# Optimization experiments

Hardware: AMD Instinct MI355X
Metric: run time of the kernel (lower is better)

Reference implementation:

```python
import jax, jax.numpy as jnp
import numpy as np

N_FOOD = 50000
N_NUT = 50000
E = 800000
D = 128      # embedding_dim == hidden_dim
H = 4        # heads
C = D // H   # per-head channels
L = 2        # num_layers
NEG_SLOPE = 0.2


def _gat_conv(x_src, x_dst, ei, Wsrc, Wdst, a_src, a_dst, bias, n_dst):
    """PyG GATConv (bipartite, no self loops, concat heads, no edge_dim)."""
    hs = (x_src @ Wsrc).reshape(-1, H, C)   # [Ns, H, C]
    hd = (x_dst @ Wdst).reshape(-1, H, C)   # [Nd, H, C]
    src, dst = ei[0], ei[1]
    alpha_s = jnp.einsum('nhc,hc->nh', hs, a_src)  # [Ns, H]
    alpha_d = jnp.einsum('nhc,hc->nh', hd, a_dst)  # [Nd, H]
    e = alpha_s[src] + alpha_d[dst]                # [E, H]
    e = jax.nn.leaky_relu(e, NEG_SLOPE)
    # segment softmax over edges grouped by destination node
    emax = jax.ops.segment_max(e, dst, num_segments=n_dst)
    emax = jnp.where(jnp.isfinite(emax), emax, 0.0)
    ex = jnp.exp(e - emax[dst])
    denom = jax.ops.segment_sum(ex, dst, num_segments=n_dst)
    alpha = ex / (denom[dst] + 1e-16)              # [E, H]
    msg = hs[src] * alpha[:, :, None]              # [E, H, C]
    out = jax.ops.segment_sum(msg, dst, num_segments=n_dst)
    return out.reshape(n_dst, H * C) + bias


def setup_inputs() -> dict:
    key = jax.random.key(0)
    ks = jax.random.split(key, 16)
    w = 1.0 / np.sqrt(D)
    a = 1.0 / np.sqrt(C)
    inp = {
        'x_food': jax.random.normal(ks[0], (N_FOOD, D), jnp.float32),
        'x_nut': jax.random.normal(ks[1], (N_NUT, D), jnp.float32),
        'Wsrc_fn': jax.random.normal(ks[2], (L, D, D), jnp.float32) * w,
        'Wdst_fn': jax.random.normal(ks[3], (L, D, D), jnp.float32) * w,
        'att_src_fn': jax.random.normal(ks[4], (L, H, C), jnp.float32) * a,
        'att_dst_fn': jax.random.normal(ks[5], (L, H, C), jnp.float32) * a,
        'bias_fn': jnp.zeros((L, D), jnp.float32),
        'Wsrc_nf': jax.random.normal(ks[6], (L, D, D), jnp.float32) * w,
        'Wdst_nf': jax.random.normal(ks[7], (L, D, D), jnp.float32) * w,
        'att_src_nf': jax.random.normal(ks[8], (L, H, C), jnp.float32) * a,
        'att_dst_nf': jax.random.normal(ks[9], (L, H, C), jnp.float32) * a,
        'bias_nf': jnp.zeros((L, D), jnp.float32),
        'ei_fn': jax.random.randint(ks[10], (2, E), 0, N_FOOD, jnp.int32),  # food -> nutrient
        'ei_nf': jax.random.randint(ks[11], (2, E), 0, N_NUT, jnp.int32),   # nutrient -> food
    }
    return inp


def reference(x_food, x_nut, Wsrc_fn, Wdst_fn, att_src_fn, att_dst_fn, bias_fn,
              Wsrc_nf, Wdst_nf, att_src_nf, att_dst_nf, bias_nf, ei_fn, ei_nf):
    h_food, h_nut = x_food, x_nut
    for l in range(L):
        # relation food --contains--> nutrient (dst = nutrient)
        out_nut = _gat_conv(h_food, h_nut, ei_fn, Wsrc_fn[l], Wdst_fn[l],
                            att_src_fn[l], att_dst_fn[l], bias_fn[l], N_NUT)
        # relation nutrient --contained_in--> food (dst = food)
        out_food = _gat_conv(h_nut, h_food, ei_nf, Wsrc_nf[l], Wdst_nf[l],
                             att_src_nf[l], att_dst_nf[l], bias_nf[l], N_FOOD)
        # dropout is identity at inference; ELU activation
        h_food = jax.nn.elu(out_food)
        h_nut = jax.nn.elu(out_nut)
    return jnp.stack([h_food, h_nut])  # [2, 50000, 128]
```

## Files before the change

### kernel.cpp

```cpp
#include <hip/hip_runtime.h>
#include <math.h>

#define NNODE 50000
#define NEDGE 800000
#define DIM   128
#define NHEAD 4
#define NTILE ((NNODE + 63) / 64)
#define NBUCK 196
#define ECHUNK 196
#define CAP   6144
#define LOG2E 1.44269504088896340736f

typedef __bf16 bf16x8 __attribute__((ext_vector_type(8)));
typedef float  f32x4  __attribute__((ext_vector_type(4)));
typedef float  f32x2  __attribute__((ext_vector_type(2)));

static __device__ __forceinline__ void bfsplit(float x, ushort& hi, ushort& lo) {
    __bf16 h = (__bf16)x;
    float hf = (float)h;
    __bf16 l = (__bf16)(x - hf);
    hi = __builtin_bit_cast(unsigned short, h);
    lo = __builtin_bit_cast(unsigned short, l);
}
static __device__ __forceinline__ ushort f2h(float x) {
    _Float16 h = (_Float16)x;
    return __builtin_bit_cast(unsigned short, h);
}
static __device__ __forceinline__ f32x2 up2v(unsigned u) {
    f32x2 r;
    r.x = (float)__builtin_bit_cast(_Float16, (unsigned short)(u & 0xffff));
    r.y = (float)__builtin_bit_cast(_Float16, (unsigned short)(u >> 16));
    return r;
}
static __device__ __forceinline__ unsigned encf(float f) {
    unsigned u = __builtin_bit_cast(unsigned, f);
    return (u >> 31) ? ~u : (u | 0x80000000u);
}
static __device__ __forceinline__ float decf(unsigned x) {
    unsigned u = (x >> 31) ? (x & 0x7fffffffu) : ~x;
    return __builtin_bit_cast(float, u);
}

__global__ __launch_bounds__(256) void bhist(const int* __restrict__ eA,
                                             const int* __restrict__ eB,
                                             int* __restrict__ bcnt) {
    int rel = (int)(blockIdx.x >= ECHUNK);
    const int* dstrow = (rel ? eB : eA) + NEDGE;
    int blk = blockIdx.x - rel * ECHUNK;
    __shared__ int hist[256];
    hist[threadIdx.x] = 0;
    __syncthreads();
    int base = blk * 4096;
    #pragma unroll
    for (int k = 0; k < 16; k++) {
        int e = base + k * 256 + threadIdx.x;
        if (e < NEDGE) atomicAdd(&hist[dstrow[e] >> 8], 1);
    }
    __syncthreads();
    int h = hist[threadIdx.x];
    if (h) atomicAdd(&bcnt[rel * 256 + threadIdx.x], h);
}

__global__ __launch_bounds__(256) void bscan(const int* __restrict__ bcnt,
                                             int* __restrict__ bko, int* __restrict__ bcur,
                                             int* __restrict__ ptrA, int* __restrict__ ptrB) {
    int rel = blockIdx.x;
    __shared__ int tmp[256];
    int t = threadIdx.x;
    int v = bcnt[rel * 256 + t];
    tmp[t] = v; __syncthreads();
    for (int off = 1; off < 256; off <<= 1) {
        int a = (t >= off) ? tmp[t - off] : 0; __syncthreads();
        tmp[t] += a; __syncthreads();
    }
    int excl = tmp[t] - v;
    bko[rel * 256 + t] = excl;
    bcur[rel * 256 + t] = excl;
    if (t == 255) (rel ? ptrB : ptrA)[NNODE] = tmp[255];
}

__global__ __launch_bounds__(256) void bscatter(const int* __restrict__ eA,
                                                const int* __restrict__ eB,
                                                int* __restrict__ bcur,
                                                unsigned* __restrict__ bktA,
                                                unsigned* __restrict__ bktB) {
    int rel = (int)(blockIdx.x >= ECHUNK);
    const int* ebase = rel ? eB : eA;
    unsigned* bkt = rel ? bktB : bktA;
    int blk = blockIdx.x - rel * ECHUNK;
    __shared__ int hist[256], bas[256], cur[256];
    hist[threadIdx.x] = 0;
    __syncthreads();
    int base = blk * 4096;
    #pragma unroll
    for (int k = 0; k < 16; k++) {
        int e = base + k * 256 + threadIdx.x;
        if (e < NEDGE) atomicAdd(&hist[ebase[NEDGE + e] >> 8], 1);
    }
    __syncthreads();
    int h = hist[threadIdx.x];
    bas[threadIdx.x] = h ? atomicAdd(&bcur[rel * 256 + threadIdx.x], h) : 0;
    cur[threadIdx.x] = 0;
    __syncthreads();
    #pragma unroll
    for (int k = 0; k < 16; k++) {
        int e = base + k * 256 + threadIdx.x;
        if (e < NEDGE) {
            int s = ebase[e], d = ebase[NEDGE + e];
            int b = d >> 8;
            int loc = atomicAdd(&cur[b], 1);
            bkt[bas[b] + loc] = ((unsigned)(d & 255) << 16) | (unsigned)s;
        }
    }
}

__global__ __launch_bounds__(256) void bsort(const unsigned* __restrict__ bktA,
                                             const unsigned* __restrict__ bktB,
                                             const int* __restrict__ bko,
                                             int* __restrict__ ptrA, int* __restrict__ ptrB,
                                             ushort* __restrict__ srcA, ushort* __restrict__ srcB) {
    int rel = (int)(blockIdx.x >= NBUCK);
    const unsigned* bkt = rel ? bktB : bktA;
    int* ptr   = rel ? ptrB : ptrA;
    ushort* srcs = rel ? srcB : srcA;
    int b = blockIdx.x - rel * NBUCK;
    int beg = bko[rel * 256 + b], end = bko[rel * 256 + b + 1];
    int cnt_e = end - beg;
    __shared__ int hist[256], excl[256], cur[256];
    __shared__ unsigned sorted[CAP];
    int t = threadIdx.x;
    hist[t] = 0;
    __syncthreads();
    for (int i = t; i < cnt_e; i += 256) atomicAdd(&hist[bkt[beg + i] >> 16], 1);
    __syncthreads();
    int v = hist[t];
    excl[t] = v; __syncthreads();
    for (int off = 1; off < 256; off <<= 1) {
        int a = (t >= off) ? excl[t - off] : 0; __syncthreads();
        excl[t] += a; __syncthreads();
    }
    int ex = excl[t] - v;
    int d = b * 256 + t;
    if (d < NNODE) ptr[d] = beg + ex;
    cur[t] = ex;
    __syncthreads();
    for (int i = t; i < cnt_e; i += 256) {
        unsigned u = bkt[beg + i];
        int dl = u >> 16;
        int p = atomicAdd(&cur[dl], 1);
        if (p < CAP) sorted[p] = u;
        else srcs[beg + p] = (ushort)(u & 0xffffu);
    }
    __syncthreads();
    int lim = cnt_e < CAP ? cnt_e : CAP;
    for (int i = t; i < lim; i += 256) {
        unsigned u = sorted[i];
        srcs[beg + i] = (ushort)(u & 0xffffu);
    }
}

__global__ void prep_wav(const float* __restrict__ Wsrc_fn, const float* __restrict__ a_src_fn,
                         const float* __restrict__ Wdst_fn, const float* __restrict__ a_dst_fn,
                         const float* __restrict__ Wsrc_nf, const float* __restrict__ a_src_nf,
                         const float* __restrict__ Wdst_nf, const float* __restrict__ a_dst_nf,
                         float* __restrict__ wav) {
    int call = blockIdx.x;
    int layer = call >> 1, which = call & 1;
    const float* Ws = which ? Wsrc_nf : Wsrc_fn;
    const float* as = which ? a_src_nf : a_src_fn;
    const float* Wd = which ? Wdst_fn : Wdst_nf;
    const float* ad = which ? a_dst_fn : a_dst_nf;
    Ws += layer * DIM * DIM; Wd += layer * DIM * DIM;
    as += layer * DIM; ad += layer * DIM;
    for (int it = threadIdx.x; it < 512; it += 256) {
        int k = it >> 2, h = it & 3;
        float s = 0.f, dv = 0.f;
        #pragma unroll 8
        for (int c = 0; c < 32; c++) {
            s  += Ws[k * DIM + h * 32 + c] * as[h * 32 + c];
            dv += Wd[k * DIM + h * 32 + c] * ad[h * 32 + c];
        }
        float* o = wav + (size_t)call * DIM * 8 + k * 8;
        o[h] = s; o[h + 4] = dv;
    }
}

__global__ __launch_bounds__(256, 3) void transform_kernel(
    const float* __restrict__ XA, const float* __restrict__ WA, const float* __restrict__ wavA,
    ushort* __restrict__ HSA, float* __restrict__ ASA, float* __restrict__ ADA,
    const float* __restrict__ XB, const float* __restrict__ WB, const float* __restrict__ wavB,
    ushort* __restrict__ HSB, float* __restrict__ ASB, float* __restrict__ ADB,
    unsigned* __restrict__ Mg, int nb)
{
    int rel = (int)(blockIdx.x >= (unsigned)nb);
    const float* X  = rel ? XB : XA;
    const float* W  = rel ? WB : WA;
    const float* wav = rel ? wavB : wavA;
    ushort* HS = rel ? HSB : HSA;
    float*  AS = rel ? ASB : ASA;
    float*  AD = rel ? ADB : ADA;

    __shared__ ushort WTh[64][136], WTl[64][136];
    __shared__ ushort wavTh[16][136], wavTl[16][136];
    __shared__ ushort hsb[64][72];
    __shared__ unsigned mloc[4];

    int vb = blockIdx.x - rel * nb;
    int half = vb & 1;
    int ch = half * 64;

    for (int i = threadIdx.x; i < 64 * DIM; i += 256) {
        int col = i & 63, k = i >> 6;
        ushort hi, lo; bfsplit(W[k * DIM + ch + col], hi, lo);
        WTh[col][k] = hi; WTl[col][k] = lo;
    }
    if (half == 0) {
        for (int i = threadIdx.x; i < 16 * DIM; i += 256) {
            int c = i & 15, k = i >> 4;
            float w = (c < 8) ? wav[k * 8 + c] : 0.f;
            ushort hi, lo; bfsplit(w, hi, lo);
            wavTh[c][k] = hi; wavTl[c][k] = lo;
        }
    }
    if (threadIdx.x < 4) mloc[threadIdx.x] = 0;
    __syncthreads();

    const int wv = threadIdx.x >> 6, lane = threadIdx.x & 63;
    const int lm = lane & 15, lq = lane >> 4;
    const int r0 = wv * 16;
    const int tstride = nb >> 1;

    auto loadX = [&](int tile, float4* dst) {
        int myrow = tile * 64 + r0 + lm;
        int rowc = myrow < NNODE ? myrow : NNODE - 1;
        const float4* Xr = (const float4*)(X + (size_t)rowc * DIM);
        #pragma unroll
        for (int kc = 0; kc < 4; kc++) {
            dst[kc * 2]     = Xr[kc * 8 + lq * 2];
            dst[kc * 2 + 1] = Xr[kc * 8 + lq * 2 + 1];
        }
    };

    auto computeTile = [&](const float4* xv, int tile) {
        int row0 = tile * 64;
        f32x4 acc[4] = {{0,0,0,0},{0,0,0,0},{0,0,0,0},{0,0,0,0}};
        f32x4 accv = {0,0,0,0};
        #pragma unroll
        for (int kc = 0; kc < 4; kc++) {
            const float* fp = (const float*)&xv[kc * 2];
            bf16x8 ah, al;
            #pragma unroll
            for (int j = 0; j < 8; j++) {
                float x = fp[j];
                __bf16 h = (__bf16)x;
                ah[j] = h;
                al[j] = (__bf16)(x - (float)h);
            }
            int k0 = kc * 32 + lq * 8;
            #pragma unroll
            for (int ct = 0; ct < 4; ct++) {
                bf16x8 bh = *(const bf16x8*)&WTh[ct * 16 + lm][k0];
                bf16x8 bl = *(const bf16x8*)&WTl[ct * 16 + lm][k0];
                acc[ct] = __builtin_amdgcn_mfma_f32_16x16x32_bf16(al, bh, acc[ct], 0, 0, 0);
                acc[ct] = __builtin_amdgcn_mfma_f32_16x16x32_bf16(ah, bl, acc[ct], 0, 0, 0);
                acc[ct] = __builtin_amdgcn_mfma_f32_16x16x32_bf16(ah, bh, acc[ct], 0, 0, 0);
            }
            if (half == 0) {
                bf16x8 vh = *(const bf16x8*)&wavTh[lm][k0];
                bf16x8 vl = *(const bf16x8*)&wavTl[lm][k0];
                accv = __builtin_amdgcn_mfma_f32_16x16x32_bf16(al, vh, accv, 0, 0, 0);
                accv = __builtin_amdgcn_mfma_f32_16x16x32_bf16(ah, vl, accv, 0, 0, 0);
                accv = __builtin_amdgcn_mfma_f32_16x16x32_bf16(ah, vh, accv, 0, 0, 0);
            }
        }

        if (half == 0 && lm < 8) {
            accv *= LOG2E;
            float mx4 = -INFINITY;
            #pragma unroll
            for (int r = 0; r < 4; r++) {
                int row = row0 + r0 + lq * 4 + r;
                if (row < NNODE) {
                    if (lm < 4) AS[row * 4 + lm] = accv[r];
                    else        AD[row * 4 + (lm - 4)] = accv[r];
                }
                mx4 = fmaxf(mx4, accv[r]);
            }
            if (lm < 4) atomicMax(&mloc[lm], encf(mx4));
        }

        __syncthreads();
        #pragma unroll
        for (int ct = 0; ct < 4; ct++) {
            #pragma unroll
            for (int r = 0; r < 4; r++)
                hsb[r0 + lq * 4 + r][ct * 16 + lm] = f2h(acc[ct][r]);
        }
        __syncthreads();
        #pragma unroll
        for (int p = 0; p < 2; p++) {
            int idx = p * 256 + (int)threadIdx.x;
            int lr = idx >> 3, off = (idx & 7) * 8;
            int rg = row0 + lr;
            if (rg < NNODE)
                *(uint4*)(HS + (size_t)rg * DIM + ch + off) = *(const uint4*)&hsb[lr][off];
        }
    };

    float4 xa[8], xb[8];
    int tile = vb >> 1;
    loadX(tile, xa);
    while (tile < NTILE) {
        if (tile + tstride < NTILE) loadX(tile + tstride, xb);
        computeTile(xa, tile);
        tile += tstride;
        if (tile >= NTILE) break;
        if (tile + tstride < NTILE) loadX(tile + tstride, xa);
        computeTile(xb, tile);
        tile += tstride;
    }

    __syncthreads();
    if (half == 0 && threadIdx.x < 4)
        atomicMax(&Mg[rel * 4 + threadIdx.x], mloc[threadIdx.x]);
}

__global__ __launch_bounds__(256) void agg_kernel(
    const ushort* __restrict__ HSA, const float* __restrict__ ASA, const float* __restrict__ ADA,
    const int* __restrict__ ptrA, const ushort* __restrict__ srcA,
    const float* __restrict__ biasA, float* __restrict__ outA,
    const ushort* __restrict__ HSB, const float* __restrict__ ASB, const float* __restrict__ ADB,
    const int* __restrict__ ptrB, const ushort* __restrict__ srcB,
    const float* __restrict__ biasB, float* __restrict__ outB,
    const unsigned* __restrict__ Mg, int nb)
{
    int rel = (int)(blockIdx.x >= (unsigned)nb);
    const uint4* HS4 = (const uint4*)(rel ? HSB : HSA);
    const float* AS = rel ? ASB : ASA;
    const float* AD = rel ? ADB : ADA;
    const ushort* srcs = rel ? srcB : srcA;
    const int* ptr = rel ? ptrB : ptrA;
    const float* bias = rel ? biasB : biasA;
    float* out = rel ? outB : outA;

    int bid = blockIdx.x - rel * nb;
    int wave = threadIdx.x >> 6, lane = threadIdx.x & 63;
    int d = bid * 4 + wave;
    if (d >= NNODE) return;

    int q  = lane >> 4;
    int li = lane & 15;
    int hh = li >> 2;

    float ad_h = AD[d * 4 + hh];
    float mm = decf(Mg[rel * 4 + hh]) + ad_h;
    mm = mm > 0.f ? mm : 0.2f * mm;

    int e0 = ptr[d], e1 = ptr[d + 1];

    float acc[8] = {0.f,0.f,0.f,0.f,0.f,0.f,0.f,0.f};
    float l = 0.f;

    int e = e0;
    for (; e + 8 <= e1; e += 8) {
        int iA = e + q, iB = e + 4 + q;
        int sA = srcs[iA], sB = srcs[iB];
        uint4 hA = HS4[sA * 16 + li];
        uint4 hB = HS4[sB * 16 + li];
        float aA = AS[sA * 4 + hh];
        float aB = AS[sB * 4 + hh];
        float vA = aA + ad_h; vA = fmaxf(vA, 0.2f * vA);
        float vB = aB + ad_h; vB = fmaxf(vB, 0.2f * vB);
        float pA = __builtin_amdgcn_exp2f(vA - mm);
        float pB = __builtin_amdgcn_exp2f(vB - mm);
        l += pA + pB;
        #pragma unroll
        for (int j = 0; j < 4; j++) {
            f32x2 h2A = up2v(((const unsigned*)&hA)[j]);
            f32x2 h2B = up2v(((const unsigned*)&hB)[j]);
            acc[2*j]   += h2A.x * pA + h2B.x * pB;
            acc[2*j+1] += h2A.y * pA + h2B.y * pB;
        }
    }
    for (; e < e1; e += 4) {
        int ee = e + q;
        bool act = ee < e1;
        int eidx = act ? ee : e1 - 1;
        int s = srcs[eidx];
        uint4 hv = HS4[s * 16 + li];
        float av = AS[s * 4 + hh];
        float v = av + ad_h; v = fmaxf(v, 0.2f * v);
        float p = __builtin_amdgcn_exp2f(v - mm);
        p = act ? p : 0.f;
        l += p;
        #pragma unroll
        for (int j = 0; j < 4; j++) {
            f32x2 h2 = up2v(((const unsigned*)&hv)[j]);
            acc[2*j]   += h2.x * p;
            acc[2*j+1] += h2.y * p;
        }
    }

    #pragma unroll
    for (int j = 0; j < 8; j++) {
        acc[j] += __shfl_xor(acc[j], 16, 64);
        acc[j] += __shfl_xor(acc[j], 32, 64);
    }
    l += __shfl_xor(l, 16, 64);
    l += __shfl_xor(l, 32, 64);

    if (q == 0) {
        float inv = 1.f / (l + 1e-16f);
        const float4* b4 = (const float4*)bias + li * 2;
        float4 b0 = b4[0], b1 = b4[1];
        float o[8];
        o[0] = acc[0] * inv + b0.x; o[1] = acc[1] * inv + b0.y;
        o[2] = acc[2] * inv + b0.z; o[3] = acc[3] * inv + b0.w;
        o[4] = acc[4] * inv + b1.x; o[5] = acc[5] * inv + b1.y;
        o[6] = acc[6] * inv + b1.z; o[7] = acc[7] * inv + b1.w;
        #pragma unroll
        for (int j = 0; j < 8; j++)
            o[j] = o[j] > 0.f ? o[j] : __expf(o[j]) - 1.f;
        float4* o4 = (float4*)(out + (size_t)d * DIM) + li * 2;
        o4[0] = make_float4(o[0], o[1], o[2], o[3]);
        o4[1] = make_float4(o[4], o[5], o[6], o[7]);
    }
}

extern "C" void kernel_launch(void* const* d_in, const int* in_sizes, int n_in,
                              void* d_out, int out_size, void* d_ws, size_t ws_size,
                              hipStream_t stream) {
    const float* x_food      = (const float*)d_in[0];
    const float* x_nut       = (const float*)d_in[1];
    const float* Wsrc_fn     = (const float*)d_in[2];
    const float* Wdst_fn     = (const float*)d_in[3];
    const float* att_src_fn  = (const float*)d_in[4];
    const float* att_dst_fn  = (const float*)d_in[5];
    const float* bias_fn     = (const float*)d_in[6];
    const float* Wsrc_nf     = (const float*)d_in[7];
    const float* Wdst_nf     = (const float*)d_in[8];
    const float* att_src_nf  = (const float*)d_in[9];
    const float* att_dst_nf  = (const float*)d_in[10];
    const float* bias_nf     = (const float*)d_in[11];
    const int*   ei_fn       = (const int*)d_in[12];
    const int*   ei_nf       = (const int*)d_in[13];
    float* out = (float*)d_out;

    char* ws = (char*)d_ws;
    size_t off = 0;
    auto alloc_f = [&](size_t n) { float* p = (float*)(ws + off); off += n * 4; return p; };
    auto alloc_i = [&](size_t n) { int* p = (int*)(ws + off); off += n * 4; return p; };
    auto alloc_u = [&](size_t n) { ushort* p = (ushort*)(ws + off); off += n * 2; return p; };

    float* B_food = alloc_f((size_t)NNODE * DIM);
    float* B_nut  = alloc_f((size_t)NNODE * DIM);
    ushort* HS_fn = alloc_u((size_t)NNODE * DIM);
    ushort* HS_nf = alloc_u((size_t)NNODE * DIM);
    float* AS_fn  = alloc_f(NNODE * NHEAD);
    float* AS_nf  = alloc_f(NNODE * NHEAD);
    float* AD_fn  = alloc_f(NNODE * NHEAD);
    float* AD_nf  = alloc_f(NNODE * NHEAD);
    float* wav    = alloc_f(4 * DIM * 8);
    int* ptr_fn   = alloc_i(50004);
    int* ptr_nf   = alloc_i(50004);
    ushort* srcs_fn = alloc_u(NEDGE);
    ushort* srcs_nf = alloc_u(NEDGE);
    int* bcnt     = alloc_i(512);
    unsigned* Mbuf = (unsigned*)alloc_i(16);
    int* bko      = alloc_i(512);
    int* bcur     = alloc_i(512);
    unsigned* bkt_fn = (unsigned*)B_food;
    unsigned* bkt_nf = (unsigned*)B_nut;

    hipMemsetAsync(bcnt, 0, (512 + 16) * 4, stream);
    bhist<<<2 * ECHUNK, 256, 0, stream>>>(ei_fn, ei_nf, bcnt);
    bscan<<<2, 256, 0, stream>>>(bcnt, bko, bcur, ptr_fn, ptr_nf);
    bscatter<<<2 * ECHUNK, 256, 0, stream>>>(ei_fn, ei_nf, bcur, bkt_fn, bkt_nf);
    bsort<<<2 * NBUCK, 256, 0, stream>>>(bkt_fn, bkt_nf, bko, ptr_fn, ptr_nf,
                                         srcs_fn, srcs_nf);

    prep_wav<<<4, 256, 0, stream>>>(Wsrc_fn, att_src_fn, Wdst_fn, att_dst_fn,
                                    Wsrc_nf, att_src_nf, Wdst_nf, att_dst_nf, wav);

    const int WL = DIM * DIM;
    const int TNB = 384;
    const int ANB = (NNODE + 3) / 4;
    float* wav0 = wav;
    float* wav1 = wav + DIM * 8;
    float* wav2 = wav + 2 * DIM * 8;
    float* wav3 = wav + 3 * DIM * 8;

    transform_kernel<<<2 * TNB, 256, 0, stream>>>(
        x_food, Wsrc_fn, wav0, HS_fn, AS_fn, AD_nf,
        x_nut,  Wsrc_nf, wav1, HS_nf, AS_nf, AD_fn, Mbuf, TNB);
    agg_kernel<<<2 * ANB, 256, 0, stream>>>(
        HS_fn, AS_fn, AD_fn, ptr_fn, srcs_fn, bias_fn, B_nut,
        HS_nf, AS_nf, AD_nf, ptr_nf, srcs_nf, bias_nf, B_food, Mbuf, ANB);

    transform_kernel<<<2 * TNB, 256, 0, stream>>>(
        B_food, Wsrc_fn + WL, wav2, HS_fn, AS_fn, AD_nf,
        B_nut,  Wsrc_nf + WL, wav3, HS_nf, AS_nf, AD_fn, Mbuf + 8, TNB);
    agg_kernel<<<2 * ANB, 256, 0, stream>>>(
        HS_fn, AS_fn, AD_fn, ptr_fn, srcs_fn, bias_fn + DIM, out + (size_t)NNODE * DIM,
        HS_nf, AS_nf, AD_nf, ptr_nf, srcs_nf, bias_nf + DIM, out, Mbuf + 8, ANB);
}
```

Before: 356.7 us.

## Split aggregation across two half-feature blocks and trim transform shared memory

The aggregation kernel now splits each destination node's 128 features into two 64-channel halves handled by separate interleaved blocks. Each wave processes 8 edges per step instead of 4, with native f16x8 conversion and FMA accumulation. The transform kernel moves the attention-vector weights from LDS into registers and halves the hsb staging buffer by writing it in two passes, which allows 4 blocks per CU and a larger grid. The split doubles gather traffic for edge indices and attention scalars and adds more barriers in the transform store path.

```diff
diff --git a/kernel.cpp b/kernel.cpp
--- a/kernel.cpp
+++ b/kernel.cpp
@@ -10,10 +10,12 @@
 #define ECHUNK 196
 #define CAP   6144
 #define LOG2E 1.44269504088896340736f
+#define NODEBLK 12500
 
 typedef __bf16 bf16x8 __attribute__((ext_vector_type(8)));
 typedef float  f32x4  __attribute__((ext_vector_type(4)));
 typedef float  f32x2  __attribute__((ext_vector_type(2)));
+typedef _Float16 f16x8 __attribute__((ext_vector_type(8)));
 
 static __device__ __forceinline__ void bfsplit(float x, ushort& hi, ushort& lo) {
     __bf16 h = (__bf16)x;
@@ -25,12 +27,6 @@
 static __device__ __forceinline__ ushort f2h(float x) {
     _Float16 h = (_Float16)x;
     return __builtin_bit_cast(unsigned short, h);
-}
-static __device__ __forceinline__ f32x2 up2v(unsigned u) {
-    f32x2 r;
-    r.x = (float)__builtin_bit_cast(_Float16, (unsigned short)(u & 0xffff));
-    r.y = (float)__builtin_bit_cast(_Float16, (unsigned short)(u >> 16));
-    return r;
 }
 static __device__ __forceinline__ unsigned encf(float f) {
     unsigned u = __builtin_bit_cast(unsigned, f);
@@ -185,7 +181,7 @@
     }
 }
 
-__global__ __launch_bounds__(256, 3) void transform_kernel(
+__global__ __launch_bounds__(256, 4) void transform_kernel(
     const float* __restrict__ XA, const float* __restrict__ WA, const float* __restrict__ wavA,
     ushort* __restrict__ HSA, float* __restrict__ ASA, float* __restrict__ ADA,
     const float* __restrict__ XB, const float* __restrict__ WB, const float* __restrict__ wavB,
@@ -201,8 +197,7 @@
     float*  AD = rel ? ADB : ADA;
 
     __shared__ ushort WTh[64][136], WTl[64][136];
-    __shared__ ushort wavTh[16][136], wavTl[16][136];
-    __shared__ ushort hsb[64][72];
+    __shared__ ushort hsb[32][72];
     __shared__ unsigned mloc[4];
 
     int vb = blockIdx.x - rel * nb;
@@ -214,21 +209,28 @@
         ushort hi, lo; bfsplit(W[k * DIM + ch + col], hi, lo);
         WTh[col][k] = hi; WTl[col][k] = lo;
     }
-    if (half == 0) {
-        for (int i = threadIdx.x; i < 16 * DIM; i += 256) {
-            int c = i & 15, k = i >> 4;
-            float w = (c < 8) ? wav[k * 8 + c] : 0.f;
-            ushort hi, lo; bfsplit(w, hi, lo);
-            wavTh[c][k] = hi; wavTl[c][k] = lo;
-        }
-    }
     if (threadIdx.x < 4) mloc[threadIdx.x] = 0;
-    __syncthreads();
 
     const int wv = threadIdx.x >> 6, lane = threadIdx.x & 63;
     const int lm = lane & 15, lq = lane >> 4;
     const int r0 = wv * 16;
     const int tstride = nb >> 1;
+
+    bf16x8 wvh[4], wvl[4];
+    if (half == 0) {
+        #pragma unroll
+        for (int kc = 0; kc < 4; kc++) {
+            int k0 = kc * 32 + lq * 8;
+            #pragma unroll
+            for (int j = 0; j < 8; j++) {
+                float w = (lm < 8) ? wav[(k0 + j) * 8 + lm] : 0.f;
+                __bf16 h = (__bf16)w;
+                wvh[kc][j] = h;
+                wvl[kc][j] = (__bf16)(w - (float)h);
+            }
+        }
+    }
+    __syncthreads();
 
     auto loadX = [&](int tile, float4* dst) {
         int myrow = tile * 64 + r0 + lm;
@@ -266,11 +268,9 @@
                 acc[ct] = __builtin_amdgcn_mfma_f32_16x16x32_bf16(ah, bh, acc[ct], 0, 0, 0);
             }
             if (half == 0) {
-                bf16x8 vh = *(const bf16x8*)&wavTh[lm][k0];
-                bf16x8 vl = *(const bf16x8*)&wavTl[lm][k0];
-                accv = __builtin_amdgcn_mfma_f32_16x16x32_bf16(al, vh, accv, 0, 0, 0);
-                accv = __builtin_amdgcn_mfma_f32_16x16x32_bf16(ah, vl, accv, 0, 0, 0);
-                accv = __builtin_amdgcn_mfma_f32_16x16x32_bf16(ah, vh, accv, 0, 0, 0);
+                accv = __builtin_amdgcn_mfma_f32_16x16x32_bf16(al, wvh[kc], accv, 0, 0, 0);
+                accv = __builtin_amdgcn_mfma_f32_16x16x32_bf16(ah, wvl[kc], accv, 0, 0, 0);
+                accv = __builtin_amdgcn_mfma_f32_16x16x32_bf16(ah, wvh[kc], accv, 0, 0, 0);
             }
         }
 
@@ -289,19 +289,20 @@
             if (lm < 4) atomicMax(&mloc[lm], encf(mx4));
         }
 
-        __syncthreads();
-        #pragma unroll
-        for (int ct = 0; ct < 4; ct++) {
-            #pragma unroll
-            for (int r = 0; r < 4; r++)
-                hsb[r0 + lq * 4 + r][ct * 16 + lm] = f2h(acc[ct][r]);
-        }
-        __syncthreads();
         #pragma unroll
         for (int p = 0; p < 2; p++) {
-            int idx = p * 256 + (int)threadIdx.x;
-            int lr = idx >> 3, off = (idx & 7) * 8;
-            int rg = row0 + lr;
+            __syncthreads();
+            if ((wv >> 1) == p) {
+                #pragma unroll
+                for (int ct = 0; ct < 4; ct++) {
+                    #pragma unroll
+                    for (int r = 0; r < 4; r++)
+                        hsb[(r0 & 31) + lq * 4 + r][ct * 16 + lm] = f2h(acc[ct][r]);
+                }
+            }
+            __syncthreads();
+            int lr = (int)threadIdx.x >> 3, off = ((int)threadIdx.x & 7) * 8;
+            int rg = row0 + p * 32 + lr;
             if (rg < NNODE)
                 *(uint4*)(HS + (size_t)rg * DIM + ch + off) = *(const uint4*)&hsb[lr][off];
         }
@@ -332,9 +333,14 @@
     const ushort* __restrict__ HSB, const float* __restrict__ ASB, const float* __restrict__ ADB,
     const int* __restrict__ ptrB, const ushort* __restrict__ srcB,
     const float* __restrict__ biasB, float* __restrict__ outB,
-    const unsigned* __restrict__ Mg, int nb)
+    const unsigned* __restrict__ Mg)
 {
-    int rel = (int)(blockIdx.x >= (unsigned)nb);
+    unsigned idx = blockIdx.x;
+    int g   = (idx >> 2) & 1;
+    int sub = (int)((idx >> 3) << 2) | (int)(idx & 3);
+    int rel = (int)(sub >= NODEBLK);
+    int bid = sub - rel * NODEBLK;
+
     const uint4* HS4 = (const uint4*)(rel ? HSB : HSA);
     const float* AS = rel ? ASB : ASA;
     const float* AD = rel ? ADB : ADA;
@@ -343,75 +349,84 @@
     const float* bias = rel ? biasB : biasA;
     float* out = rel ? outB : outA;
 
-    int bid = blockIdx.x - rel * nb;
     int wave = threadIdx.x >> 6, lane = threadIdx.x & 63;
     int d = bid * 4 + wave;
-    if (d >= NNODE) return;
-
-    int q  = lane >> 4;
-    int li = lane & 15;
-    int hh = li >> 2;
+
+    int q  = lane >> 3;
+    int li = lane & 7;
+    int hh = g * 2 + (li >> 2);
 
     float ad_h = AD[d * 4 + hh];
     float mm = decf(Mg[rel * 4 + hh]) + ad_h;
-    mm = mm > 0.f ? mm : 0.2f * mm;
+    mm = fmaxf(mm, 0.2f * mm);
 
     int e0 = ptr[d], e1 = ptr[d + 1];
 
     float acc[8] = {0.f,0.f,0.f,0.f,0.f,0.f,0.f,0.f};
     float l = 0.f;
+    int rowoff = g * 8 + li;
 
     int e = e0;
-    for (; e + 8 <= e1; e += 8) {
-        int iA = e + q, iB = e + 4 + q;
-        int sA = srcs[iA], sB = srcs[iB];
-        uint4 hA = HS4[sA * 16 + li];
-        uint4 hB = HS4[sB * 16 + li];
-        float aA = AS[sA * 4 + hh];
-        float aB = AS[sB * 4 + hh];
+    for (; e + 16 <= e1; e += 16) {
+        int sA = srcs[e + q], sB = srcs[e + 8 + q];
+        uint4 uA = HS4[sA * 16 + rowoff];
+        uint4 uB = HS4[sB * 16 + rowoff];
+        float aA = AS[sA * 4 + hh], aB = AS[sB * 4 + hh];
         float vA = aA + ad_h; vA = fmaxf(vA, 0.2f * vA);
         float vB = aB + ad_h; vB = fmaxf(vB, 0.2f * vB);
         float pA = __builtin_amdgcn_exp2f(vA - mm);
         float pB = __builtin_amdgcn_exp2f(vB - mm);
         l += pA + pB;
-        #pragma unroll
-        for (int j = 0; j < 4; j++) {
-            f32x2 h2A = up2v(((const unsigned*)&hA)[j]);
-            f32x2 h2B = up2v(((const unsigned*)&hB)[j]);
-            acc[2*j]   += h2A.x * pA + h2B.x * pB;
-            acc[2*j+1] += h2A.y * pA + h2B.y * pB;
-        }
-    }
-    for (; e < e1; e += 4) {
+        f16x8 hA = __builtin_bit_cast(f16x8, uA);
+        f16x8 hB = __builtin_bit_cast(f16x8, uB);
+        #pragma unroll
+        for (int j = 0; j < 8; j++) {
+            acc[j] = __builtin_fmaf((float)hA[j], pA, acc[j]);
+            acc[j] = __builtin_fmaf((float)hB[j], pB, acc[j]);
+        }
+    }
+    for (; e + 8 <= e1; e += 8) {
+        int s = srcs[e + q];
+        uint4 u = HS4[s * 16 + rowoff];
+        float a = AS[s * 4 + hh];
+        float v = a + ad_h; v = fmaxf(v, 0.2f * v);
+        float p = __builtin_amdgcn_exp2f(v - mm);
+        l += p;
+        f16x8 h = __builtin_bit_cast(f16x8, u);
+        #pragma unroll
+        for (int j = 0; j < 8; j++)
+            acc[j] = __builtin_fmaf((float)h[j], p, acc[j]);
+    }
+    if (e < e1) {
         int ee = e + q;
         bool act = ee < e1;
         int eidx = act ? ee : e1 - 1;
         int s = srcs[eidx];
-        uint4 hv = HS4[s * 16 + li];
-        float av = AS[s * 4 + hh];
-        float v = av + ad_h; v = fmaxf(v, 0.2f * v);
+        uint4 u = HS4[s * 16 + rowoff];
+        float a = AS[s * 4 + hh];
+        float v = a + ad_h; v = fmaxf(v, 0.2f * v);
         float p = __builtin_amdgcn_exp2f(v - mm);
         p = act ? p : 0.f;
         l += p;
-        #pragma unroll
-        for (int j = 0; j < 4; j++) {
-            f32x2 h2 = up2v(((const unsigned*)&hv)[j]);
-            acc[2*j]   += h2.x * p;
-            acc[2*j+1] += h2.y * p;
-        }
+        f16x8 h = __builtin_bit_cast(f16x8, u);
+        #pragma unroll
+        for (int j = 0; j < 8; j++)
+            acc[j] = __builtin_fmaf((float)h[j], p, acc[j]);
     }
 
     #pragma unroll
     for (int j = 0; j < 8; j++) {
+        acc[j] += __shfl_xor(acc[j], 8, 64);
         acc[j] += __shfl_xor(acc[j], 16, 64);
         acc[j] += __shfl_xor(acc[j], 32, 64);
     }
+    l += __shfl_xor(l, 8, 64);
     l += __shfl_xor(l, 16, 64);
     l += __shfl_xor(l, 32, 64);
 
     if (q == 0) {
         float inv = 1.f / (l + 1e-16f);
-        const float4* b4 = (const float4*)bias + li * 2;
+        const float4* b4 = (const float4*)(bias + g * 64) + li * 2;
         float4 b0 = b4[0], b1 = b4[1];
         float o[8];
         o[0] = acc[0] * inv + b0.x; o[1] = acc[1] * inv + b0.y;
@@ -421,7 +436,7 @@
         #pragma unroll
         for (int j = 0; j < 8; j++)
             o[j] = o[j] > 0.f ? o[j] : __expf(o[j]) - 1.f;
-        float4* o4 = (float4*)(out + (size_t)d * DIM) + li * 2;
+        float4* o4 = (float4*)(out + (size_t)d * DIM + g * 64) + li * 2;
         o4[0] = make_float4(o[0], o[1], o[2], o[3]);
         o4[1] = make_float4(o[4], o[5], o[6], o[7]);
     }
@@ -483,8 +498,8 @@
                                     Wsrc_nf, att_src_nf, Wdst_nf, att_dst_nf, wav);
 
     const int WL = DIM * DIM;
-    const int TNB = 384;
-    const int ANB = (NNODE + 3) / 4;
+    const int TNB = 512;
+    const int AGRID = 2 * 2 * NODEBLK;
     float* wav0 = wav;
     float* wav1 = wav + DIM * 8;
     float* wav2 = wav + 2 * DIM * 8;
@@ -493,14 +508,14 @@
     transform_kernel<<<2 * TNB, 256, 0, stream>>>(
         x_food, Wsrc_fn, wav0, HS_fn, AS_fn, AD_nf,
         x_nut,  Wsrc_nf, wav1, HS_nf, AS_nf, AD_fn, Mbuf, TNB);
-    agg_kernel<<<2 * ANB, 256, 0, stream>>>(
+    agg_kernel<<<AGRID, 256, 0, stream>>>(
         HS_fn, AS_fn, AD_fn, ptr_fn, srcs_fn, bias_fn, B_nut,
-        HS_nf, AS_nf, AD_nf, ptr_nf, srcs_nf, bias_nf, B_food, Mbuf, ANB);
+        HS_nf, AS_nf, AD_nf, ptr_nf, srcs_nf, bias_nf, B_food, Mbuf);
 
     transform_kernel<<<2 * TNB, 256, 0, stream>>>(
         B_food, Wsrc_fn + WL, wav2, HS_fn, AS_fn, AD_nf,
         B_nut,  Wsrc_nf + WL, wav3, HS_nf, AS_nf, AD_fn, Mbuf + 8, TNB);
-    agg_kernel<<<2 * ANB, 256, 0, stream>>>(
+    agg_kernel<<<AGRID, 256, 0, stream>>>(
         HS_fn, AS_fn, AD_fn, ptr_fn, srcs_fn, bias_fn + DIM, out + (size_t)NNODE * DIM,
-        HS_nf, AS_nf, AD_nf, ptr_nf, srcs_nf, bias_nf + DIM, out, Mbuf + 8, ANB);
-}
+        HS_nf, AS_nf, AD_nf, ptr_nf, srcs_nf, bias_nf + DIM, out, Mbuf + 8);
+}
```

Result: slower. 440.9 us (+23.6%).
